# Kernel optimization log

Measured on AMD Instinct MI355X. Metric: run time of the kernel, lower is better.

## Reference

```python
import jax, jax.numpy as jnp
import numpy as np

O, D, E, K, H, A = 1024, 1024, 16, 4, 2048, 64  # option_dim, obs_dim, num_experts, k, moe_hidden, act_dim
LOSS_COEF = 0.01


def cv_squared(x):
    # torch .var() is unbiased (ddof=1)
    eps = 1e-10
    return jnp.var(x, ddof=1) / (jnp.mean(x) ** 2 + eps)


def setup_inputs() -> dict:
    key = jax.random.key(0)
    ks = jax.random.split(key, 8)
    s = 0.02
    return {
        "obs": jax.random.normal(ks[0], (O, D), jnp.float32),
        # original inits w_gate to zeros (degenerate top-k); use small random for a meaningful baseline
        "w_gate": jax.random.normal(ks[1], (O, D, E), jnp.float32) * s,
        "w1": jax.random.normal(ks[2], (E, D, H), jnp.float32) * s,   # expert MLP layer 1
        "b1": jnp.zeros((E, H), jnp.float32),
        "w2": jax.random.normal(ks[3], (E, H, A), jnp.float32) * s,   # expert MLP layer 2
        "b2": jnp.zeros((E, A), jnp.float32),
        "last_w": jax.random.normal(ks[4], (O, D, A), jnp.float32),   # last_w_layer
        "last_b": jax.random.normal(ks[5], (O, A), jnp.float32),      # last_b_layer
    }


def reference(obs, w_gate, w1, b1, w2, b2, last_w, last_b):
    # ---- noisy_top_k_gating (this version applies no noise) ----
    logits = jnp.einsum('od,ode->oe', obs, w_gate)                    # [O, E]
    top_vals, top_idx = jax.lax.top_k(logits, K + 1)
    topk_gates = jax.nn.softmax(top_vals[:, :K], axis=1)              # softmax over top-k logits
    rows = jnp.arange(O)[:, None]
    gates = jnp.zeros_like(logits).at[rows, top_idx[:, :K]].set(topk_gates)  # scatter -> [O, E]
    importance = gates.sum(axis=1)
    load = (gates > 0).sum(axis=1).astype(jnp.float32)                # faithful to original (sum over dim 1)
    loss = (cv_squared(importance) + cv_squared(load)) * LOSS_COEF
    # ---- dispatch / expert MLPs / combine (dense-over-experts equivalent; zero gates kill non-top-k) ----
    h = jax.nn.relu(jnp.einsum('od,edh->oeh', obs, w1) + b1[None])    # [O, E, H]
    y = jnp.einsum('oe,oeh,eha->oa', gates, h, w2) + gates @ b2       # [O, A]
    # ---- action head ----
    mu = jnp.einsum('od,oda->oa', obs, last_w) + last_b               # [O, A]
    action_probs = jax.nn.softmax(mu, axis=-1)
    z = (action_probs == 0.0).astype(action_probs.dtype) * 1e-08
    log_action_probs = jnp.log(action_probs + z)
    return (action_probs, log_action_probs, y, loss)
```

## Files before the change

kernel.cpp:

```cpp
#include <hip/hip_runtime.h>
#include <hip/hip_bf16.h>
#include <math.h>

#define O_ 1024
#define D_ 1024
#define E_ 16
#define K_ 4
#define H_ 2048
#define A_ 64
#define LOSS_COEF 0.01f

#define FLT_MIN_NORMAL 1.17549435e-38f

using floatx4 = __attribute__((ext_vector_type(4))) float;
using fragb   = __attribute__((ext_vector_type(8))) short;

static __device__ __forceinline__ ushort f2bf(float f) {
    unsigned u = __builtin_bit_cast(unsigned, f);
    u += 0x7fffu + ((u >> 16) & 1u);
    return (ushort)(u >> 16);
}

__global__ __launch_bounds__(256) void gating_kernel(
    const float* __restrict__ obs, const float* __restrict__ w_gate,
    int* __restrict__ topk_idx, float* __restrict__ topk_gate,
    float* __restrict__ imp, float* __restrict__ loadv)
{
    const int o = blockIdx.x;
    const int t = threadIdx.x;
    __shared__ float xs[D_];
    __shared__ float part[64][20];
    __shared__ float logits[E_];

    const float4* xrow = (const float4*)(obs + (size_t)o * D_);
    for (int i = t; i < D_ / 4; i += 256) ((float4*)xs)[i] = xrow[i];
    __syncthreads();

    const int dg = t >> 2, e4 = t & 3;
    const float4* wg = (const float4*)(w_gate + (size_t)o * (D_ * E_));
    float4 acc = make_float4(0.f, 0.f, 0.f, 0.f);
    #pragma unroll 4
    for (int i = 0; i < 16; ++i) {
        int d = dg + (i << 6);
        float4 w = wg[d * 4 + e4];
        float x = xs[d];
        acc.x += x * w.x; acc.y += x * w.y; acc.z += x * w.z; acc.w += x * w.w;
    }
    *(float4*)&part[dg][e4 * 4] = acc;
    __syncthreads();
    if (t < E_) {
        float s = 0.f;
        for (int g = 0; g < 64; ++g) s += part[g][t];
        logits[t] = s;
    }
    __syncthreads();
    if (t == 0) {
        float lv[E_];
        #pragma unroll
        for (int i = 0; i < E_; ++i) lv[i] = logits[i];
        int idx[K_]; float val[K_];
        bool used[E_] = {};
        for (int k = 0; k < K_; ++k) {
            int bi = 0; float bv = -INFINITY;
            for (int i = 0; i < E_; ++i)
                if (!used[i] && lv[i] > bv) { bv = lv[i]; bi = i; }
            used[bi] = true; idx[k] = bi; val[k] = bv;
        }
        float m = val[0];
        float ex[K_]; float s = 0.f;
        for (int k = 0; k < K_; ++k) { ex[k] = expf(val[k] - m); s += ex[k]; }
        float inv = 1.f / s;
        float sumg = 0.f; int ld = 0;
        for (int k = 0; k < K_; ++k) {
            float g = ex[k] * inv;
            topk_idx[o * K_ + k] = idx[k];
            topk_gate[o * K_ + k] = g;
            sumg += g;
            if (g > 0.f) ld++;
        }
        imp[o] = sumg;
        loadv[o] = (float)ld;
    }
}

__global__ void zero_cnt_kernel(int* __restrict__ cnt)
{
    if (threadIdx.x < E_) cnt[threadIdx.x] = 0;
}

__global__ __launch_bounds__(256) void build_dispatch_kernel(
    const int* __restrict__ topk_idx, const float* __restrict__ topk_gate,
    int* __restrict__ cnt, int* __restrict__ rows, float* __restrict__ gatev)
{
    int i = blockIdx.x * 256 + threadIdx.x;
    int e = topk_idx[i];
    int pos = atomicAdd(&cnt[e], 1);
    rows[e * O_ + pos] = i >> 2;
    gatev[e * O_ + pos] = topk_gate[i];
}

__global__ __launch_bounds__(64) void y_init_kernel(
    const int* __restrict__ topk_idx, const float* __restrict__ topk_gate,
    const float* __restrict__ b2, float* __restrict__ y)
{
    int o = blockIdx.x, a = threadIdx.x;
    float acc = 0.f;
    #pragma unroll
    for (int k = 0; k < K_; ++k) {
        int e = topk_idx[o * K_ + k];
        acc += topk_gate[o * K_ + k] * b2[e * A_ + a];
    }
    y[(size_t)o * A_ + a] = acc;
}

__global__ __launch_bounds__(1024) void loss_kernel(
    const float* __restrict__ imp, const float* __restrict__ loadv,
    float* __restrict__ out_loss)
{
    __shared__ float s1[1024], s2[1024];
    __shared__ float mean1, mean2;
    int t = threadIdx.x;
    float a = imp[t], b = loadv[t];
    s1[t] = a; s2[t] = b; __syncthreads();
    for (int s = 512; s > 0; s >>= 1) {
        if (t < s) { s1[t] += s1[t + s]; s2[t] += s2[t + s]; }
        __syncthreads();
    }
    if (t == 0) { mean1 = s1[0] / O_; mean2 = s2[0] / O_; }
    __syncthreads();
    float d1 = a - mean1, d2 = b - mean2;
    s1[t] = d1 * d1; s2[t] = d2 * d2; __syncthreads();
    for (int s = 512; s > 0; s >>= 1) {
        if (t < s) { s1[t] += s1[t + s]; s2[t] += s2[t + s]; }
        __syncthreads();
    }
    if (t == 0) {
        float var1 = s1[0] / (O_ - 1), var2 = s2[0] / (O_ - 1);
        const float eps = 1e-10f;
        out_loss[0] = (var1 / (mean1 * mean1 + eps) + var2 / (mean2 * mean2 + eps)) * LOSS_COEF;
    }
}

__global__ __launch_bounds__(256) void cvt_obs_kernel(
    const float* __restrict__ src, ushort* __restrict__ dst)
{
    int i = blockIdx.x * 256 + threadIdx.x;
    float4 v = ((const float4*)src)[i];
    ushort4 u;
    u.x = f2bf(v.x); u.y = f2bf(v.y); u.z = f2bf(v.z); u.w = f2bf(v.w);
    ((ushort4*)dst)[i] = u;
}

__global__ __launch_bounds__(256) void transpose_bf16_kernel(
    const float* __restrict__ src, ushort* __restrict__ dst, int R, int C)
{
    const int c0 = blockIdx.x * 64, r0 = blockIdx.y * 64, e = blockIdx.z;
    __shared__ ushort tile[64][72];
    const float* s = src + (size_t)e * R * C;
    const int t = threadIdx.x;
    const int rr = t >> 4, cq = t & 15;
    #pragma unroll
    for (int i = 0; i < 4; ++i) {
        int r = rr + i * 16;
        float4 v = *(const float4*)(s + (size_t)(r0 + r) * C + c0 + cq * 4);
        ushort4 u;
        u.x = f2bf(v.x); u.y = f2bf(v.y); u.z = f2bf(v.z); u.w = f2bf(v.w);
        *(ushort4*)&tile[r][cq * 4] = u;
    }
    __syncthreads();
    ushort* dbase = dst + (size_t)e * R * C;
    const int cc = t >> 4, rq = t & 15;
    #pragma unroll
    for (int i = 0; i < 4; ++i) {
        int c = cc + i * 16;
        ushort4 u;
        u.x = tile[rq * 4 + 0][c];
        u.y = tile[rq * 4 + 1][c];
        u.z = tile[rq * 4 + 2][c];
        u.w = tile[rq * 4 + 3][c];
        *(ushort4*)(dbase + (size_t)(c0 + c) * R + r0 + rq * 4) = u;
    }
}

__global__ __launch_bounds__(256) void expert_mfma_kernel(
    const ushort* __restrict__ obs_bf, const ushort* __restrict__ w1T,
    const float* __restrict__ b1, const ushort* __restrict__ w2T,
    const int* __restrict__ cnt, const int* __restrict__ rows,
    const float* __restrict__ gatev, float* __restrict__ y)
{
    const int ht = blockIdx.x, rt = blockIdx.y, e = blockIdx.z;
    const int n = cnt[e];
    if (rt * 64 >= n) return;
    const int t = threadIdx.x, wv = t >> 6, l = t & 63;
    const int lm = l & 15, q = l >> 4;

    __shared__ int   rid[64];
    __shared__ float rgate[64];
    __shared__ float b1s[64];
    __shared__ ushort Hs[64][72];

    if (t < 64) {
        int gi = rt * 64 + t;
        rid[t]   = (gi < n) ? rows[e * O_ + gi]  : -1;
        rgate[t] = (gi < n) ? gatev[e * O_ + gi] : 0.f;
        b1s[t]   = b1[e * H_ + ht * 64 + t];
    }
    __syncthreads();

    int arow = rid[wv * 16 + lm]; if (arow < 0) arow = 0;
    const ushort* ap = obs_bf + (size_t)arow * D_ + q * 8;
    const ushort* bp = w1T + ((size_t)(e * H_ + ht * 64 + lm)) * D_ + q * 8;

    floatx4 acc[4] = {};
    #pragma unroll 2
    for (int k0 = 0; k0 < D_; k0 += 32) {
        fragb a  = *(const fragb*)(ap + k0);
        fragb b0 = *(const fragb*)(bp + k0);
        fragb b1f = *(const fragb*)(bp + 16 * D_ + k0);
        fragb b2f = *(const fragb*)(bp + 32 * D_ + k0);
        fragb b3f = *(const fragb*)(bp + 48 * D_ + k0);
        acc[0] = __builtin_amdgcn_mfma_f32_16x16x32_bf16(a, b0,  acc[0], 0, 0, 0);
        acc[1] = __builtin_amdgcn_mfma_f32_16x16x32_bf16(a, b1f, acc[1], 0, 0, 0);
        acc[2] = __builtin_amdgcn_mfma_f32_16x16x32_bf16(a, b2f, acc[2], 0, 0, 0);
        acc[3] = __builtin_amdgcn_mfma_f32_16x16x32_bf16(a, b3f, acc[3], 0, 0, 0);
    }

    const int r0 = wv * 16 + q * 4;
    #pragma unroll
    for (int nt = 0; nt < 4; ++nt) {
        int col = nt * 16 + lm;
        float bb = b1s[col];
        #pragma unroll
        for (int r = 0; r < 4; ++r) {
            float h = acc[nt][r] + bb;
            h = h > 0.f ? h : 0.f;
            Hs[r0 + r][col] = f2bf(h * rgate[r0 + r]);
        }
    }
    __syncthreads();

    const ushort* hp = &Hs[wv * 16 + lm][q * 8];
    const ushort* wp = w2T + ((size_t)(e * A_ + lm)) * H_ + ht * 64 + q * 8;
    floatx4 acc2[4] = {};
    #pragma unroll
    for (int k = 0; k < 2; ++k) {
        fragb a = *(const fragb*)(hp + k * 32);
        #pragma unroll
        for (int nt = 0; nt < 4; ++nt) {
            fragb b = *(const fragb*)(wp + (size_t)nt * 16 * H_ + k * 32);
            acc2[nt] = __builtin_amdgcn_mfma_f32_16x16x32_bf16(a, b, acc2[nt], 0, 0, 0);
        }
    }

    #pragma unroll
    for (int r = 0; r < 4; ++r) {
        int orow = rid[r0 + r];
        if (orow >= 0) {
            #pragma unroll
            for (int nt = 0; nt < 4; ++nt)
                atomicAdd(&y[(size_t)orow * A_ + nt * 16 + lm], acc2[nt][r]);
        }
    }
}

__global__ __launch_bounds__(256) void action_head_kernel(
    const float* __restrict__ obs, const float* __restrict__ last_w,
    const float* __restrict__ last_b,
    float* __restrict__ probs, float* __restrict__ logprobs)
{
    const int o = blockIdx.x;
    const int t = threadIdx.x;
    __shared__ float xs[D_];
    __shared__ float red[16][A_];

    const float4* xrow = (const float4*)(obs + (size_t)o * D_);
    for (int i = t; i < D_ / 4; i += 256) ((float4*)xs)[i] = xrow[i];
    __syncthreads();

    const int a4 = t & 15, dg = t >> 4;
    const float* lw = last_w + (size_t)o * (D_ * A_);
    float acc0 = 0.f, acc1 = 0.f, acc2 = 0.f, acc3 = 0.f;
    #pragma unroll 8
    for (int i = 0; i < D_ / 16; ++i) {
        int d = dg + (i << 4);
        float4 w = *(const float4*)(lw + (size_t)d * A_ + a4 * 4);
        float x = xs[d];
        acc0 += x * w.x; acc1 += x * w.y; acc2 += x * w.z; acc3 += x * w.w;
    }
    *(float4*)&red[dg][a4 * 4] = make_float4(acc0, acc1, acc2, acc3);
    __syncthreads();

    if (t < A_) {
        float mu = last_b[(size_t)o * A_ + t];
        #pragma unroll
        for (int g = 0; g < 16; ++g) mu += red[g][t];
        float mx = mu;
        #pragma unroll
        for (int off = 32; off > 0; off >>= 1) mx = fmaxf(mx, __shfl_xor(mx, off, 64));
        float ex = expf(mu - mx);
        if (ex < FLT_MIN_NORMAL) ex = 0.f;
        float s = ex;
        #pragma unroll
        for (int off = 32; off > 0; off >>= 1) s += __shfl_xor(s, off, 64);
        float p = ex / s;
        if (p < FLT_MIN_NORMAL) p = 0.f;
        probs[(size_t)o * A_ + t] = p;
        float z = (p == 0.f) ? 1e-8f : 0.f;
        logprobs[(size_t)o * A_ + t] = logf(p + z);
    }
}

extern "C" void kernel_launch(void* const* d_in, const int* in_sizes, int n_in,
                              void* d_out, int out_size, void* d_ws, size_t ws_size,
                              hipStream_t stream)
{
    const float* obs    = (const float*)d_in[0];
    const float* w_gate = (const float*)d_in[1];
    const float* w1     = (const float*)d_in[2];
    const float* b1     = (const float*)d_in[3];
    const float* w2     = (const float*)d_in[4];
    const float* b2     = (const float*)d_in[5];
    const float* last_w = (const float*)d_in[6];
    const float* last_b = (const float*)d_in[7];

    float* out   = (float*)d_out;
    float* probs = out;
    float* logp  = out + O_ * A_;
    float* yout  = out + 2 * O_ * A_;
    float* loss  = out + 3 * O_ * A_;

    char* ws = (char*)d_ws;
    int*    topk_idx  = (int*)(ws);
    float*  topk_gate = (float*)(ws + (16 << 10));
    float*  imp       = (float*)(ws + (32 << 10));
    float*  loadv     = (float*)(ws + (36 << 10));
    int*    cnt       = (int*)(ws + (40 << 10));
    int*    rows      = (int*)(ws + (41 << 10));
    float*  gatev     = (float*)(ws + (105 << 10));
    ushort* obs_bf    = (ushort*)(ws + (256 << 10));
    ushort* w1T       = (ushort*)(ws + (256 << 10) + (2 << 20));
    ushort* w2T       = (ushort*)(ws + (256 << 10) + (66 << 20));

    hipLaunchKernelGGL(zero_cnt_kernel, dim3(1), dim3(64), 0, stream, cnt);
    hipLaunchKernelGGL(gating_kernel, dim3(O_), dim3(256), 0, stream,
                       obs, w_gate, topk_idx, topk_gate, imp, loadv);
    hipLaunchKernelGGL(build_dispatch_kernel, dim3((O_ * K_) / 256), dim3(256), 0, stream,
                       topk_idx, topk_gate, cnt, rows, gatev);
    hipLaunchKernelGGL(y_init_kernel, dim3(O_), dim3(A_), 0, stream,
                       topk_idx, topk_gate, b2, yout);
    hipLaunchKernelGGL(loss_kernel, dim3(1), dim3(1024), 0, stream, imp, loadv, loss);

    hipLaunchKernelGGL(cvt_obs_kernel, dim3((O_ * D_) / 1024), dim3(256), 0, stream,
                       obs, obs_bf);
    hipLaunchKernelGGL(transpose_bf16_kernel, dim3(H_ / 64, D_ / 64, E_), dim3(256), 0, stream,
                       w1, w1T, D_, H_);
    hipLaunchKernelGGL(transpose_bf16_kernel, dim3(A_ / 64, H_ / 64, E_), dim3(256), 0, stream,
                       w2, w2T, H_, A_);

    hipLaunchKernelGGL(expert_mfma_kernel, dim3(H_ / 64, O_ / 64, E_), dim3(256), 0, stream,
                       obs_bf, w1T, b1, w2T, cnt, rows, gatev, yout);
    hipLaunchKernelGGL(action_head_kernel, dim3(O_), dim3(256), 0, stream,
                       obs, last_w, last_b, probs, logp);
}
```

Baseline: 690.3 us.

## Retile expert MFMA kernel to 128x128 with LDS double buffering

Rewrites the expert GEMM to use 128x128 block tiles with a 2x2 wave layout. A and B are staged into XOR-swizzled LDS through async global_load_lds, double-buffered over 64-wide K chunks. Previously every fragment was read directly from global memory with little reuse. This raises operand reuse and overlaps loads with MFMA, at the cost of 64KB+ LDS per block, fewer blocks, and more padding waste for experts whose row count is not a multiple of 128.

```diff
diff --git a/kernel.cpp b/kernel.cpp
--- a/kernel.cpp
+++ b/kernel.cpp
@@ -19,6 +19,12 @@
     unsigned u = __builtin_bit_cast(unsigned, f);
     u += 0x7fffu + ((u >> 16) & 1u);
     return (ushort)(u >> 16);
+}
+
+static __device__ __forceinline__ void gld_lds16(const void* g, void* l) {
+    __builtin_amdgcn_global_load_lds(
+        (const __attribute__((address_space(1))) void*)g,
+        (__attribute__((address_space(3))) void*)l, 16, 0, 0);
 }
 
 __global__ __launch_bounds__(256) void gating_kernel(
@@ -182,7 +188,7 @@
     }
 }
 
-__global__ __launch_bounds__(256) void expert_mfma_kernel(
+__global__ __launch_bounds__(256, 2) void expert_mfma_kernel(
     const ushort* __restrict__ obs_bf, const ushort* __restrict__ w1T,
     const float* __restrict__ b1, const ushort* __restrict__ w2T,
     const int* __restrict__ cnt, const int* __restrict__ rows,
@@ -190,75 +196,122 @@
 {
     const int ht = blockIdx.x, rt = blockIdx.y, e = blockIdx.z;
     const int n = cnt[e];
-    if (rt * 64 >= n) return;
+    if (rt * 128 >= n) return;
+
     const int t = threadIdx.x, wv = t >> 6, l = t & 63;
     const int lm = l & 15, q = l >> 4;
-
-    __shared__ int   rid[64];
-    __shared__ float rgate[64];
-    __shared__ float b1s[64];
-    __shared__ ushort Hs[64][72];
-
-    if (t < 64) {
-        int gi = rt * 64 + t;
-        rid[t]   = (gi < n) ? rows[e * O_ + gi]  : -1;
-        rgate[t] = (gi < n) ? gatev[e * O_ + gi] : 0.f;
-        b1s[t]   = b1[e * H_ + ht * 64 + t];
-    }
-    __syncthreads();
-
-    int arow = rid[wv * 16 + lm]; if (arow < 0) arow = 0;
-    const ushort* ap = obs_bf + (size_t)arow * D_ + q * 8;
-    const ushort* bp = w1T + ((size_t)(e * H_ + ht * 64 + lm)) * D_ + q * 8;
-
-    floatx4 acc[4] = {};
-    #pragma unroll 2
-    for (int k0 = 0; k0 < D_; k0 += 32) {
-        fragb a  = *(const fragb*)(ap + k0);
-        fragb b0 = *(const fragb*)(bp + k0);
-        fragb b1f = *(const fragb*)(bp + 16 * D_ + k0);
-        fragb b2f = *(const fragb*)(bp + 32 * D_ + k0);
-        fragb b3f = *(const fragb*)(bp + 48 * D_ + k0);
-        acc[0] = __builtin_amdgcn_mfma_f32_16x16x32_bf16(a, b0,  acc[0], 0, 0, 0);
-        acc[1] = __builtin_amdgcn_mfma_f32_16x16x32_bf16(a, b1f, acc[1], 0, 0, 0);
-        acc[2] = __builtin_amdgcn_mfma_f32_16x16x32_bf16(a, b2f, acc[2], 0, 0, 0);
-        acc[3] = __builtin_amdgcn_mfma_f32_16x16x32_bf16(a, b3f, acc[3], 0, 0, 0);
-    }
-
-    const int r0 = wv * 16 + q * 4;
-    #pragma unroll
-    for (int nt = 0; nt < 4; ++nt) {
-        int col = nt * 16 + lm;
-        float bb = b1s[col];
+    const int wr = wv >> 1, wc = wv & 1;
+
+    __shared__ __align__(16) ushort smem[32768];
+    __shared__ int   rid_s[128];
+    __shared__ float rgate_s[128];
+    __shared__ float b1s[128];
+
+    if (t < 128) {
+        int gi = rt * 128 + t;
+        rid_s[t]   = (gi < n) ? rows[e * O_ + gi]  : -1;
+        rgate_s[t] = (gi < n) ? gatev[e * O_ + gi] : 0.f;
+    } else {
+        b1s[t - 128] = b1[e * H_ + ht * 128 + (t - 128)];
+    }
+    __syncthreads();
+
+    const int swe = ((l & 7) ^ (l >> 3)) << 3;
+    const ushort* asrc[4];
+    const ushort* bsrc[4];
+    #pragma unroll
+    for (int j = 0; j < 4; ++j) {
+        int r = (j * 4 + wv) * 8 + (l >> 3);
+        int arow = rid_s[r]; if (arow < 0) arow = 0;
+        asrc[j] = obs_bf + (size_t)arow * D_ + swe;
+        bsrc[j] = w1T + ((size_t)(e * H_ + ht * 128 + r)) * D_ + swe;
+    }
+
+    auto stage = [&](int b, int kc) {
+        ushort* ab_ = &smem[b * 8192];
+        ushort* bb_ = &smem[16384 + b * 8192];
+        const int ko = kc * 64;
+        #pragma unroll
+        for (int j = 0; j < 4; ++j) {
+            gld_lds16(asrc[j] + ko, ab_ + (j * 4 + wv) * 512);
+            gld_lds16(bsrc[j] + ko, bb_ + (j * 4 + wv) * 512);
+        }
+    };
+
+    floatx4 acc[4][4] = {};
+    int buf = 0;
+    stage(0, 0);
+    __syncthreads();
+
+    for (int kc = 0; kc < 16; ++kc) {
+        if (kc < 15) stage(buf ^ 1, kc + 1);
+        const ushort* ab = &smem[buf * 8192];
+        const ushort* bb = &smem[16384 + buf * 8192];
+        #pragma unroll
+        for (int ks = 0; ks < 2; ++ks) {
+            const int co = ((ks * 4 + q) ^ (lm & 7)) << 3;
+            fragb a[4];
+            #pragma unroll
+            for (int i = 0; i < 4; ++i)
+                a[i] = *(const fragb*)(ab + (wr * 64 + i * 16 + lm) * 64 + co);
+            #pragma unroll
+            for (int nt = 0; nt < 4; ++nt) {
+                fragb b = *(const fragb*)(bb + (wc * 64 + nt * 16 + lm) * 64 + co);
+                #pragma unroll
+                for (int i = 0; i < 4; ++i)
+                    acc[i][nt] = __builtin_amdgcn_mfma_f32_16x16x32_bf16(a[i], b, acc[i][nt], 0, 0, 0);
+            }
+        }
+        __syncthreads();
+        buf ^= 1;
+    }
+
+    ushort* Hs = smem;
+    #pragma unroll
+    for (int i = 0; i < 4; ++i) {
+        #pragma unroll
+        for (int nt = 0; nt < 4; ++nt) {
+            const int col = wc * 64 + nt * 16 + lm;
+            const float bb = b1s[col];
+            #pragma unroll
+            for (int r = 0; r < 4; ++r) {
+                const int row = wr * 64 + i * 16 + q * 4 + r;
+                float h = acc[i][nt][r] + bb;
+                h = h > 0.f ? h : 0.f;
+                Hs[row * 136 + col] = f2bf(h * rgate_s[row]);
+            }
+        }
+    }
+    __syncthreads();
+
+    floatx4 acc2[4][2] = {};
+    #pragma unroll
+    for (int ks = 0; ks < 4; ++ks) {
+        fragb a[4];
+        #pragma unroll
+        for (int i = 0; i < 4; ++i)
+            a[i] = *(const fragb*)(Hs + (wr * 64 + i * 16 + lm) * 136 + ks * 32 + q * 8);
+        #pragma unroll
+        for (int nt = 0; nt < 2; ++nt) {
+            const int acol = wc * 32 + nt * 16 + lm;
+            fragb b = *(const fragb*)(w2T + ((size_t)(e * A_ + acol)) * H_ + ht * 128 + ks * 32 + q * 8);
+            #pragma unroll
+            for (int i = 0; i < 4; ++i)
+                acc2[i][nt] = __builtin_amdgcn_mfma_f32_16x16x32_bf16(a[i], b, acc2[i][nt], 0, 0, 0);
+        }
+    }
+
+    #pragma unroll
+    for (int i = 0; i < 4; ++i) {
         #pragma unroll
         for (int r = 0; r < 4; ++r) {
-            float h = acc[nt][r] + bb;
-            h = h > 0.f ? h : 0.f;
-            Hs[r0 + r][col] = f2bf(h * rgate[r0 + r]);
-        }
-    }
-    __syncthreads();
-
-    const ushort* hp = &Hs[wv * 16 + lm][q * 8];
-    const ushort* wp = w2T + ((size_t)(e * A_ + lm)) * H_ + ht * 64 + q * 8;
-    floatx4 acc2[4] = {};
-    #pragma unroll
-    for (int k = 0; k < 2; ++k) {
-        fragb a = *(const fragb*)(hp + k * 32);
-        #pragma unroll
-        for (int nt = 0; nt < 4; ++nt) {
-            fragb b = *(const fragb*)(wp + (size_t)nt * 16 * H_ + k * 32);
-            acc2[nt] = __builtin_amdgcn_mfma_f32_16x16x32_bf16(a, b, acc2[nt], 0, 0, 0);
-        }
-    }
-
-    #pragma unroll
-    for (int r = 0; r < 4; ++r) {
-        int orow = rid[r0 + r];
-        if (orow >= 0) {
-            #pragma unroll
-            for (int nt = 0; nt < 4; ++nt)
-                atomicAdd(&y[(size_t)orow * A_ + nt * 16 + lm], acc2[nt][r]);
+            const int row = wr * 64 + i * 16 + q * 4 + r;
+            const int orow = rid_s[row];
+            if (orow >= 0) {
+                #pragma unroll
+                for (int nt = 0; nt < 2; ++nt)
+                    atomicAdd(&y[(size_t)orow * A_ + wc * 32 + nt * 16 + lm], acc2[i][nt][r]);
+            }
         }
     }
 }
@@ -357,7 +410,7 @@
     hipLaunchKernelGGL(transpose_bf16_kernel, dim3(A_ / 64, H_ / 64, E_), dim3(256), 0, stream,
                        w2, w2T, H_, A_);
 
-    hipLaunchKernelGGL(expert_mfma_kernel, dim3(H_ / 64, O_ / 64, E_), dim3(256), 0, stream,
+    hipLaunchKernelGGL(expert_mfma_kernel, dim3(H_ / 128, O_ / 128, E_), dim3(256), 0, stream,
                        obs_bf, w1T, b1, w2T, cnt, rows, gatev, yout);
     hipLaunchKernelGGL(action_head_kernel, dim3(O_), dim3(256), 0, stream,
                        obs, last_w, last_b, probs, logp);
```

Measured after the change: 571.5 us. 1.21x faster.
